# Optimization experiments

Hardware: AMD Instinct MI355X
Metric: run time of the kernel (lower is better)

## Reference

```python
import jax, jax.numpy as jnp
import numpy as np

B, T, C, H, Wimg = 16, 6, 4, 420, 312
PH, PW = 14, 12
E = 768
GH, GW = H // PH, Wimg // PW  # 30, 26 -> 780 patches
N_VALID = 390


def setup_inputs() -> dict:
    key = jax.random.key(0)
    kx, kw, kb = jax.random.split(key, 3)
    x = jax.random.normal(kx, (B, T, C, H, Wimg), dtype=jnp.float32)
    W = jax.random.normal(kw, (E, C, PH, PW), dtype=jnp.float32) * 0.02
    b = jax.random.normal(kb, (E,), dtype=jnp.float32) * 0.02
    # static patch mask: keep half the patches (unique, sorted indices like torch.nonzero)
    rng = np.random.default_rng(0)
    valid = np.sort(rng.choice(GH * GW, size=N_VALID, replace=False)).astype(np.int32)
    return {"x": x, "W": W, "b": b, "valid_indices": jnp.asarray(valid)}


def reference(x, W, b, valid_indices):
    Bv, Tv, Cv, Hv, Wv = x.shape
    Ev, _, ph, pw = W.shape
    gh, gw = Hv // ph, Wv // pw
    # non-overlapping stride=kernel conv == patchify + GEMM
    xp = x.reshape(Bv * Tv, Cv, gh, ph, gw, pw)
    out = jnp.einsum('ncipjq,ecpq->nije', xp, W) + b  # [B*T, gh, gw, E]
    out = out.reshape(Bv, Tv, gh * gw, Ev)            # [B, T, n_patches, E]
    return out[:, :, valid_indices, :]                # [B, T, n_valid, E]
```

## Files before the change

kernel.cpp:

```cpp
#include <hip/hip_runtime.h>

#define M_TOT 37440
#define N_E   768
#define K_TOT 672
#define NV    390
#define GWID  26
#define PHh   14
#define PWw   12
#define IMW   312
#define CSTRIDE 131040
#define NSTRIDE 524160

#define NKT   7
#define ROWP  104

typedef short bf16x8 __attribute__((ext_vector_type(8)));
typedef float f32x4  __attribute__((ext_vector_type(4)));
typedef unsigned short u16;
typedef u16 u16x4 __attribute__((ext_vector_type(4)));

#define A_PAD_BYTES 54512640u
#define W_PAD_BYTES 1118208u
#define WS_NEEDED   (A_PAD_BYTES + W_PAD_BYTES)

#define NBLK_A 8190
#define NBLK_W 168

static __device__ __forceinline__ u16 f2bf(float f) {
  unsigned u = __builtin_bit_cast(unsigned, f);
  u = (u + 0x7FFFu + ((u >> 16) & 1u)) >> 16;
  return (u16)u;
}

#define GLOAD_LDS16(g, l) \
  __builtin_amdgcn_global_load_lds((const __attribute__((address_space(1))) void*)(g), \
                                   (__attribute__((address_space(3))) void*)(l), 16, 0, 0)

__global__ __launch_bounds__(256) void patchify(
    const float* __restrict__ x, const float* __restrict__ w,
    const int* __restrict__ valid, u16* __restrict__ Ap, u16* __restrict__ Wp) {
  const int bid = blockIdx.x;
  const int tid = threadIdx.x;
  if (bid < NBLK_A) {
    const int g  = bid * 256 + tid;
    const int m  = g / 56;
    const int rr = g - m * 56;
    const int t  = rr >> 3, run = rr & 7;
    const int nimg = m / NV;
    const int v    = m - nimg * NV;
    const int gidx = valid[v];
    const int gi = gidx / GWID, gj = gidx - gi * GWID;
    const int c  = rr / PHh,    p  = rr - c * PHh;
    const float* src = x + (size_t)nimg * NSTRIDE + (size_t)c * CSTRIDE
                         + (size_t)(gi * PHh + p) * IMW + gj * PWw;
    f32x4 f0 = *(const f32x4*)(src + 0);
    f32x4 f1 = *(const f32x4*)(src + 4);
    f32x4 f2 = *(const f32x4*)(src + 8);
    u16* dst = Ap + ((size_t)(t * M_TOT + m)) * ROWP + run * 12;
    u16x4 h0 = {f2bf(f0.x), f2bf(f0.y), f2bf(f0.z), f2bf(f0.w)};
    u16x4 h1 = {f2bf(f1.x), f2bf(f1.y), f2bf(f1.z), f2bf(f1.w)};
    u16x4 h2 = {f2bf(f2.x), f2bf(f2.y), f2bf(f2.z), f2bf(f2.w)};
    *(u16x4*)(dst + 0) = h0;
    *(u16x4*)(dst + 4) = h1;
    *(u16x4*)(dst + 8) = h2;
  } else {
    const int g  = (bid - NBLK_A) * 256 + tid;
    const int n  = g / 56;
    const int rr = g - n * 56;
    const int t  = rr >> 3, run = rr & 7;
    const float* src = w + (size_t)n * K_TOT + rr * 12;
    f32x4 f0 = *(const f32x4*)(src + 0);
    f32x4 f1 = *(const f32x4*)(src + 4);
    f32x4 f2 = *(const f32x4*)(src + 8);
    u16* dst = Wp + ((size_t)(t * N_E + n)) * ROWP + run * 12;
    u16x4 h0 = {f2bf(f0.x), f2bf(f0.y), f2bf(f0.z), f2bf(f0.w)};
    u16x4 h1 = {f2bf(f1.x), f2bf(f1.y), f2bf(f1.z), f2bf(f1.w)};
    u16x4 h2 = {f2bf(f2.x), f2bf(f2.y), f2bf(f2.z), f2bf(f2.w)};
    *(u16x4*)(dst + 0) = h0;
    *(u16x4*)(dst + 4) = h1;
    *(u16x4*)(dst + 8) = h2;
  }
}

__global__ __launch_bounds__(256) void gemm_bf16(
    const u16* __restrict__ Ap, const u16* __restrict__ Wp,
    const float* __restrict__ bias, float* __restrict__ out) {
  __shared__ u16 lds[2][2][128 * ROWP];

  const int tid  = threadIdx.x;
  const int lane = tid & 63;
  const int wid  = tid >> 6;
  const int wr   = wid >> 1, wc = wid & 1;
  const int lrow = lane & 15, lhi = lane >> 4;

  const int n0 = blockIdx.x * 128;
  const int m0 = blockIdx.y * 128;

  auto STAGE = [&](int t, int b) {
    if (wid < 2) {
      const u16* srcb = Ap + ((size_t)(t * M_TOT + m0)) * ROWP + lane * 8;
      #pragma unroll
      for (int j = 0; j < 13; ++j) {
        const int c = wid * 13 + j;
        GLOAD_LDS16(srcb + c * 512, (char*)&lds[b][0][0] + c * 1024);
      }
    } else {
      const u16* srcb = Wp + ((size_t)(t * N_E + n0)) * ROWP + lane * 8;
      #pragma unroll
      for (int j = 0; j < 13; ++j) {
        const int c = (wid - 2) * 13 + j;
        GLOAD_LDS16(srcb + c * 512, (char*)&lds[b][1][0] + c * 1024);
      }
    }
  };

  f32x4 acc[4][4];
  #pragma unroll
  for (int i = 0; i < 4; ++i)
    #pragma unroll
    for (int j = 0; j < 4; ++j)
      acc[i][j] = (f32x4){0.f, 0.f, 0.f, 0.f};

  STAGE(0, 0);

  for (int t = 0; t < NKT; ++t) {
    const int b = t & 1;
    if (t < NKT - 1) {
      STAGE(t + 1, b ^ 1);
      asm volatile("s_waitcnt vmcnt(13)" ::: "memory");
    } else {
      asm volatile("s_waitcnt vmcnt(0)" ::: "memory");
    }
    __builtin_amdgcn_s_barrier();

    #pragma unroll
    for (int kk = 0; kk < 3; ++kk) {
      bf16x8 a[4], bfr[4];
      #pragma unroll
      for (int i = 0; i < 4; ++i)
        a[i] = *(const bf16x8*)&lds[b][0][(wr * 64 + i * 16 + lrow) * ROWP + kk * 32 + lhi * 8];
      #pragma unroll
      for (int j = 0; j < 4; ++j)
        bfr[j] = *(const bf16x8*)&lds[b][1][(wc * 64 + j * 16 + lrow) * ROWP + kk * 32 + lhi * 8];
      #pragma unroll
      for (int i = 0; i < 4; ++i)
        #pragma unroll
        for (int j = 0; j < 4; ++j)
          acc[i][j] = __builtin_amdgcn_mfma_f32_16x16x32_bf16(a[i], bfr[j], acc[i][j], 0, 0, 0);
    }
    asm volatile("" ::: "memory");
    __builtin_amdgcn_s_barrier();
  }

  float bv[4];
  #pragma unroll
  for (int j = 0; j < 4; ++j)
    bv[j] = bias[n0 + wc * 64 + j * 16 + lrow];

  #pragma unroll
  for (int i = 0; i < 4; ++i) {
    const int mbase = m0 + wr * 64 + i * 16 + lhi * 4;
    #pragma unroll
    for (int j = 0; j < 4; ++j) {
      const int e = n0 + wc * 64 + j * 16 + lrow;
      float* op = out + (size_t)mbase * N_E + e;
      #pragma unroll
      for (int tt = 0; tt < 4; ++tt) {
        if (mbase + tt < M_TOT) op[(size_t)tt * N_E] = acc[i][j][tt] + bv[j];
      }
    }
  }
}

#define ROWB 104
__global__ __launch_bounds__(256) void patch_gemm_fused(
    const float* __restrict__ x, const float* __restrict__ w,
    const float* __restrict__ bias, const int* __restrict__ valid,
    float* __restrict__ out) {
  __shared__ u16 Alds[128 * ROWB];
  __shared__ u16 Blds[128 * ROWB];
  const int tid  = threadIdx.x;
  const int lane = tid & 63;
  const int wid  = tid >> 6;
  const int wr   = wid >> 1, wc = wid & 1;
  const int lrow = lane & 15, lhi = lane >> 4;
  const int m0 = blockIdx.x * 128;
  const int n0 = blockIdx.y * 128;
  const int arow = tid & 127;
  int m = m0 + arow;
  if (m >= M_TOT) m = M_TOT - 1;
  const int nimg = m / NV;
  const int v    = m - nimg * NV;
  const int g    = valid[v];
  const int gi   = g / GWID;
  const int gj   = g - gi * GWID;
  const float* xrow = x + (size_t)nimg * NSTRIDE + (size_t)(gi * PHh) * IMW + gj * PWw;
  const int half = tid >> 7;
  const float* wrow = w + (size_t)(n0 + arow) * K_TOT;
  f32x4 acc[4][4];
  #pragma unroll
  for (int i = 0; i < 4; ++i)
    #pragma unroll
    for (int j = 0; j < 4; ++j)
      acc[i][j] = (f32x4){0.f, 0.f, 0.f, 0.f};
  for (int t = 0; t < 7; ++t) {
    #pragma unroll
    for (int it = 0; it < 4; ++it) {
      const int run = half + it * 2;
      const int rr  = t * 8 + run;
      const int c   = rr / PHh;
      const int p   = rr - c * PHh;
      const float* src = xrow + (size_t)c * CSTRIDE + p * IMW;
      f32x4 f0 = *(const f32x4*)(src + 0);
      f32x4 f1 = *(const f32x4*)(src + 4);
      f32x4 f2 = *(const f32x4*)(src + 8);
      u16x4 h0 = {f2bf(f0.x), f2bf(f0.y), f2bf(f0.z), f2bf(f0.w)};
      u16x4 h1 = {f2bf(f1.x), f2bf(f1.y), f2bf(f1.z), f2bf(f1.w)};
      u16x4 h2 = {f2bf(f2.x), f2bf(f2.y), f2bf(f2.z), f2bf(f2.w)};
      u16* dst = &Alds[arow * ROWB + run * 12];
      *(u16x4*)(dst + 0) = h0;
      *(u16x4*)(dst + 4) = h1;
      *(u16x4*)(dst + 8) = h2;
    }
    #pragma unroll
    for (int i = 0; i < 6; ++i) {
      const int col = half * 48 + i * 8;
      const float* src = wrow + t * 96 + col;
      f32x4 f0 = *(const f32x4*)(src + 0);
      f32x4 f1 = *(const f32x4*)(src + 4);
      u16x4 h0 = {f2bf(f0.x), f2bf(f0.y), f2bf(f0.z), f2bf(f0.w)};
      u16x4 h1 = {f2bf(f1.x), f2bf(f1.y), f2bf(f1.z), f2bf(f1.w)};
      u16* dst = &Blds[arow * ROWB + col];
      *(u16x4*)(dst + 0) = h0;
      *(u16x4*)(dst + 4) = h1;
    }
    __syncthreads();
    #pragma unroll
    for (int kk = 0; kk < 3; ++kk) {
      bf16x8 a[4], b[4];
      #pragma unroll
      for (int i = 0; i < 4; ++i)
        a[i] = *(const bf16x8*)&Alds[(wr * 64 + i * 16 + lrow) * ROWB + kk * 32 + lhi * 8];
      #pragma unroll
      for (int j = 0; j < 4; ++j)
        b[j] = *(const bf16x8*)&Blds[(wc * 64 + j * 16 + lrow) * ROWB + kk * 32 + lhi * 8];
      #pragma unroll
      for (int i = 0; i < 4; ++i)
        #pragma unroll
        for (int j = 0; j < 4; ++j)
          acc[i][j] = __builtin_amdgcn_mfma_f32_16x16x32_bf16(a[i], b[j], acc[i][j], 0, 0, 0);
    }
    __syncthreads();
  }
  float bv[4];
  #pragma unroll
  for (int j = 0; j < 4; ++j)
    bv[j] = bias[n0 + wc * 64 + j * 16 + lrow];
  #pragma unroll
  for (int i = 0; i < 4; ++i) {
    const int mbase = m0 + wr * 64 + i * 16 + lhi * 4;
    #pragma unroll
    for (int j = 0; j < 4; ++j) {
      const int e = n0 + wc * 64 + j * 16 + lrow;
      float* op = out + (size_t)mbase * N_E + e;
      #pragma unroll
      for (int tt = 0; tt < 4; ++tt) {
        if (mbase + tt < M_TOT) op[(size_t)tt * N_E] = acc[i][j][tt] + bv[j];
      }
    }
  }
}

extern "C" void kernel_launch(void* const* d_in, const int* in_sizes, int n_in,
                              void* d_out, int out_size, void* d_ws, size_t ws_size,
                              hipStream_t stream) {
  const float* x     = (const float*)d_in[0];
  const float* w     = (const float*)d_in[1];
  const float* b     = (const float*)d_in[2];
  const int*   valid = (const int*)d_in[3];
  float* out = (float*)d_out;

  if (ws_size >= (size_t)WS_NEEDED) {
    u16* Aws = (u16*)d_ws;
    u16* Wws = (u16*)((char*)d_ws + A_PAD_BYTES);
    patchify<<<NBLK_A + NBLK_W, 256, 0, stream>>>(x, w, valid, Aws, Wws);
    dim3 grid(N_E / 128, (M_TOT + 127) / 128);
    gemm_bf16<<<grid, dim3(256), 0, stream>>>(Aws, Wws, b, out);
  } else {
    dim3 grid((M_TOT + 127) / 128, N_E / 128);
    patch_gemm_fused<<<grid, dim3(256), 0, stream>>>(x, w, b, valid, out);
  }
}
```

Measured before the change: 422.0 us.

## Use row-major padded A/W layout, single-buffer LDS, and XCD-aware tile swizzle

The patchified A and W buffers change from k-tile-major slabs to a row-major layout, with each row holding 7 padded k-tiles of 104 elements, so a block's loads walk contiguous row segments. The GEMM drops LDS double-buffering in favour of a single buffer, raising occupancy via launch_bounds(256,3). It also launches a 1D grid whose workgroup ids are remapped per XCD so neighbouring tiles share an XCD's L2. In exchange, loads no longer overlap compute within a block, and overlap now depends on multiple resident blocks per CU.

New measurement: 384.8 us. -8.8%, faster.

```diff
diff --git a/kernel.cpp b/kernel.cpp
--- a/kernel.cpp
+++ b/kernel.cpp
@@ -12,7 +12,8 @@
 #define NSTRIDE 524160
 
 #define NKT   7
-#define ROWP  104
+#define TPAD  104
+#define ROWT  728
 
 typedef short bf16x8 __attribute__((ext_vector_type(8)));
 typedef float f32x4  __attribute__((ext_vector_type(4)));
@@ -25,6 +26,10 @@
 
 #define NBLK_A 8190
 #define NBLK_W 168
+
+#define NWG   1758
+#define SWZ_Q 219
+#define SWZ_R 6
 
 static __device__ __forceinline__ u16 f2bf(float f) {
   unsigned u = __builtin_bit_cast(unsigned, f);
@@ -56,7 +61,7 @@
     f32x4 f0 = *(const f32x4*)(src + 0);
     f32x4 f1 = *(const f32x4*)(src + 4);
     f32x4 f2 = *(const f32x4*)(src + 8);
-    u16* dst = Ap + ((size_t)(t * M_TOT + m)) * ROWP + run * 12;
+    u16* dst = Ap + (size_t)m * ROWT + t * TPAD + run * 12;
     u16x4 h0 = {f2bf(f0.x), f2bf(f0.y), f2bf(f0.z), f2bf(f0.w)};
     u16x4 h1 = {f2bf(f1.x), f2bf(f1.y), f2bf(f1.z), f2bf(f1.w)};
     u16x4 h2 = {f2bf(f2.x), f2bf(f2.y), f2bf(f2.z), f2bf(f2.w)};
@@ -72,7 +77,7 @@
     f32x4 f0 = *(const f32x4*)(src + 0);
     f32x4 f1 = *(const f32x4*)(src + 4);
     f32x4 f2 = *(const f32x4*)(src + 8);
-    u16* dst = Wp + ((size_t)(t * N_E + n)) * ROWP + run * 12;
+    u16* dst = Wp + (size_t)n * ROWT + t * TPAD + run * 12;
     u16x4 h0 = {f2bf(f0.x), f2bf(f0.y), f2bf(f0.z), f2bf(f0.w)};
     u16x4 h1 = {f2bf(f1.x), f2bf(f1.y), f2bf(f1.z), f2bf(f1.w)};
     u16x4 h2 = {f2bf(f2.x), f2bf(f2.y), f2bf(f2.z), f2bf(f2.w)};
@@ -82,10 +87,10 @@
   }
 }
 
-__global__ __launch_bounds__(256) void gemm_bf16(
+__global__ __launch_bounds__(256, 3) void gemm_bf16(
     const u16* __restrict__ Ap, const u16* __restrict__ Wp,
     const float* __restrict__ bias, float* __restrict__ out) {
-  __shared__ u16 lds[2][2][128 * ROWP];
+  __shared__ u16 lds[2][128 * TPAD];
 
   const int tid  = threadIdx.x;
   const int lane = tid & 63;
@@ -93,26 +98,34 @@
   const int wr   = wid >> 1, wc = wid & 1;
   const int lrow = lane & 15, lhi = lane >> 4;
 
-  const int n0 = blockIdx.x * 128;
-  const int m0 = blockIdx.y * 128;
-
-  auto STAGE = [&](int t, int b) {
-    if (wid < 2) {
-      const u16* srcb = Ap + ((size_t)(t * M_TOT + m0)) * ROWP + lane * 8;
-      #pragma unroll
-      for (int j = 0; j < 13; ++j) {
-        const int c = wid * 13 + j;
-        GLOAD_LDS16(srcb + c * 512, (char*)&lds[b][0][0] + c * 1024);
-      }
-    } else {
-      const u16* srcb = Wp + ((size_t)(t * N_E + n0)) * ROWP + lane * 8;
-      #pragma unroll
-      for (int j = 0; j < 13; ++j) {
-        const int c = (wid - 2) * 13 + j;
-        GLOAD_LDS16(srcb + c * 512, (char*)&lds[b][1][0] + c * 1024);
-      }
-    }
-  };
+  const int orig = blockIdx.x;
+  const int xcd = orig & 7, pos = orig >> 3;
+  const int lid = (xcd < SWZ_R ? xcd * (SWZ_Q + 1)
+                               : SWZ_R * (SWZ_Q + 1) + (xcd - SWZ_R) * SWZ_Q) + pos;
+  const int n0 = (lid % 6) * 128;
+  const int m0 = (lid / 6) * 128;
+
+  int goff[13];
+  const u16* gbase;
+  if (wid < 2) {
+    #pragma unroll
+    for (int j = 0; j < 13; ++j) {
+      const int g = (wid * 13 + j) * 64 + lane;
+      const int row = g / 13, col = g - row * 13;
+      int ar = m0 + row; if (ar > M_TOT - 1) ar = M_TOT - 1;
+      goff[j] = ar * ROWT + col * 8;
+    }
+    gbase = Ap;
+  } else {
+    #pragma unroll
+    for (int j = 0; j < 13; ++j) {
+      const int g = ((wid - 2) * 13 + j) * 64 + lane;
+      const int row = g / 13, col = g - row * 13;
+      goff[j] = (n0 + row) * ROWT + col * 8;
+    }
+    gbase = Wp;
+  }
+  char* ldst = (char*)&lds[wid >> 1][0] + (wid & 1) * (13 * 1024);
 
   f32x4 acc[4][4];
   #pragma unroll
@@ -121,35 +134,28 @@
     for (int j = 0; j < 4; ++j)
       acc[i][j] = (f32x4){0.f, 0.f, 0.f, 0.f};
 
-  STAGE(0, 0);
-
   for (int t = 0; t < NKT; ++t) {
-    const int b = t & 1;
-    if (t < NKT - 1) {
-      STAGE(t + 1, b ^ 1);
-      asm volatile("s_waitcnt vmcnt(13)" ::: "memory");
-    } else {
-      asm volatile("s_waitcnt vmcnt(0)" ::: "memory");
-    }
-    __builtin_amdgcn_s_barrier();
+    #pragma unroll
+    for (int j = 0; j < 13; ++j)
+      GLOAD_LDS16(gbase + goff[j] + t * TPAD, ldst + j * 1024);
+    __syncthreads();
 
     #pragma unroll
     for (int kk = 0; kk < 3; ++kk) {
       bf16x8 a[4], bfr[4];
       #pragma unroll
       for (int i = 0; i < 4; ++i)
-        a[i] = *(const bf16x8*)&lds[b][0][(wr * 64 + i * 16 + lrow) * ROWP + kk * 32 + lhi * 8];
+        a[i] = *(const bf16x8*)&lds[0][(wr * 64 + i * 16 + lrow) * TPAD + kk * 32 + lhi * 8];
       #pragma unroll
       for (int j = 0; j < 4; ++j)
-        bfr[j] = *(const bf16x8*)&lds[b][1][(wc * 64 + j * 16 + lrow) * ROWP + kk * 32 + lhi * 8];
+        bfr[j] = *(const bf16x8*)&lds[1][(wc * 64 + j * 16 + lrow) * TPAD + kk * 32 + lhi * 8];
       #pragma unroll
       for (int i = 0; i < 4; ++i)
         #pragma unroll
         for (int j = 0; j < 4; ++j)
           acc[i][j] = __builtin_amdgcn_mfma_f32_16x16x32_bf16(a[i], bfr[j], acc[i][j], 0, 0, 0);
     }
-    asm volatile("" ::: "memory");
-    __builtin_amdgcn_s_barrier();
+    __syncthreads();
   }
 
   float bv[4];
@@ -284,8 +290,7 @@
     u16* Aws = (u16*)d_ws;
     u16* Wws = (u16*)((char*)d_ws + A_PAD_BYTES);
     patchify<<<NBLK_A + NBLK_W, 256, 0, stream>>>(x, w, valid, Aws, Wws);
-    dim3 grid(N_E / 128, (M_TOT + 127) / 128);
-    gemm_bf16<<<grid, dim3(256), 0, stream>>>(Aws, Wws, b, out);
+    gemm_bf16<<<NWG, 256, 0, stream>>>(Aws, Wws, b, out);
   } else {
     dim3 grid((M_TOT + 127) / 128, N_E / 128);
     patch_gemm_fused<<<grid, dim3(256), 0, stream>>>(x, w, b, valid, out);
```
